# Optimization experiments

Hardware: AMD Instinct MI355X
Metric: run time of the kernel (lower is better)

The kernel has to match this reference:

```python
import jax, jax.numpy as jnp
import numpy as np

H, W, C, HEADS = 28, 28, 512, 16
N = H * W
FF = 4 * C
DH = C // HEADS
NUM_REL = (2 * H - 1) * W + (2 * W - 1) + 1  # max relative index + 1 (source table is under-sized; see notes)


def _relative_indices():
    ys, xs = np.meshgrid(np.arange(H), np.arange(W), indexing='ij')
    py, px = ys.reshape(-1), xs.reshape(-1)
    # rel[q, k] = (y_k - y_q + H) * W + (x_k - x_q + W), matching the source loop
    rel = (py[None, :] - py[:, None] + H) * W + (px[None, :] - px[:, None] + W)
    return jnp.asarray(rel, dtype=jnp.int32)  # (N, N)


def setup_inputs() -> dict:
    key = jax.random.key(0)
    ks = jax.random.split(key, 9)
    g = lambda k, shape, s: (jax.random.normal(k, shape, jnp.float32) * s)
    return {
        'x': g(ks[0], (16, C, H, W), 1.0),
        'ln_w': jnp.ones((C,), jnp.float32),
        'ln_b': jnp.zeros((C,), jnp.float32),
        'Wq': g(ks[1], (C, C), 0.02), 'bq': jnp.zeros((C,), jnp.float32),
        'Wk': g(ks[2], (C, C), 0.02), 'bk': jnp.zeros((C,), jnp.float32),
        'Wv': g(ks[3], (C, C), 0.02), 'bv': jnp.zeros((C,), jnp.float32),
        'Wo': g(ks[4], (C, C), 0.02), 'bo': jnp.zeros((C,), jnp.float32),
        'rel_bias': g(ks[5], (HEADS, NUM_REL), 0.02),
        'W1': g(ks[6], (C, FF), 0.02), 'b1': jnp.zeros((FF,), jnp.float32),
        'W2': g(ks[7], (FF, C), 0.02), 'b2': jnp.zeros((C,), jnp.float32),
        'rel_idx': _relative_indices(),
    }


def reference(x, ln_w, ln_b, Wq, bq, Wk, bk, Wv, bv, Wo, bo, rel_bias, W1, b1, W2, b2, rel_idx):
    b = x.shape[0]
    xc = jnp.transpose(x, (0, 2, 3, 1)).reshape(b, N, C)  # b n c
    # LayerNorm over channels (per spatial position)
    mu = xc.mean(-1, keepdims=True)
    var = jnp.mean(jnp.square(xc - mu), -1, keepdims=True)
    xn = (xc - mu) * jax.lax.rsqrt(var + 1e-5) * ln_w + ln_b

    split = lambda t: t.reshape(b, N, HEADS, DH).transpose(0, 2, 1, 3)  # b h n d
    q = split(xn @ Wq + bq)
    k = split(xn @ Wk + bk)
    v = split(xn @ Wv + bv)

    bias = rel_bias[:, rel_idx]  # gather -> (heads, n, n)
    scores = jnp.einsum('bhnd,bhmd->bhnm', q, k) + bias[None]  # no 1/sqrt(d), faithful to source
    attn = jax.nn.softmax(scores, axis=-1)
    out = jnp.einsum('bhnm,bhmd->bhnd', attn, v)
    out = out.transpose(0, 2, 1, 3).reshape(b, N, C) @ Wo + bo

    x1 = xc + out  # skip (Identity) + attention branch
    ff = jax.nn.gelu(x1 @ W1 + b1, approximate=False) @ W2 + b2
    x2 = x1 + ff
    return x2.reshape(b, H, W, C).transpose(0, 3, 1, 2)  # back to b c h w
```

## Files before the change

kernel.cpp:

```cpp
#include <hip/hip_runtime.h>
#include <hip/hip_bf16.h>
#include <math.h>
#include <stdint.h>


typedef __bf16 bf16;
typedef __attribute__((ext_vector_type(8))) __bf16 bf16x8;
typedef __attribute__((ext_vector_type(4))) __bf16 bf16x4;
typedef __attribute__((ext_vector_type(4))) float f32x4;

#define NN 784
#define CC 512
#define NHEADS 16
#define DHEAD 32
#define FFD 2048
#define NBATCH 16
#define NREL 1596
#define MFULL (NBATCH * NN)
#define PACKSZ ((size_t)6422528)

__global__ __launch_bounds__(256) void detect_dtype(const unsigned int* xw, int* flag)
{
  __shared__ int cnt[256];
  int plausible = 0;
  for (int i = threadIdx.x; i < 1024; i += 256) {
    unsigned w = xw[i];
    unsigned lo = w & 0xFFFFu;
    unsigned e = (lo >> 7) & 0xFFu;
    if (lo == 0u || (e >= 90u && e <= 140u)) plausible++;
  }
  cnt[threadIdx.x] = plausible;
  __syncthreads();
  if (threadIdx.x == 0) {
    int tot = 0;
    for (int i = 0; i < 256; i++) tot += cnt[i];
    flag[0] = (tot >= 768) ? 1 : 0;
  }
}


__global__ __launch_bounds__(256) void transpose_split(
    const float* __restrict__ W, bf16* __restrict__ th, bf16* __restrict__ tl,
    int K, int Nout, int roff, const int* __restrict__ flag)
{
  if (flag[0] != 0) return;
  __shared__ float tile[32][33];
  int n0 = blockIdx.x * 32, k0 = blockIdx.y * 32;
  int tx = threadIdx.x & 31, ty = threadIdx.x >> 5;
  #pragma unroll
  for (int r = 0; r < 32; r += 8)
    tile[ty + r][tx] = W[(size_t)(k0 + ty + r) * Nout + n0 + tx];
  __syncthreads();
  #pragma unroll
  for (int r = 0; r < 32; r += 8) {
    float v = tile[tx][ty + r];
    bf16 h = (bf16)v;
    float lo = v - (float)h;
    size_t idx = (size_t)(roff + n0 + ty + r) * K + k0 + tx;
    th[idx] = h;
    tl[idx] = (bf16)lo;
  }
}

__global__ __launch_bounds__(256) void ln_single(
    const float* __restrict__ x, const float* __restrict__ lnw,
    const float* __restrict__ lnb, bf16* __restrict__ xh,
    const int* __restrict__ flag)
{
  if (flag[0] != 0) return;
  int bn = blockIdx.x;
  int b = bn / NN, n = bn - b * NN;
  const float* xb = x + (size_t)b * CC * NN + n;
  int t = threadIdx.x;
  float v0 = xb[(size_t)t * NN];
  float v1 = xb[(size_t)(t + 256) * NN];
  float s = v0 + v1, ss = v0 * v0 + v1 * v1;
  #pragma unroll
  for (int m = 32; m >= 1; m >>= 1) {
    s  += __shfl_xor(s,  m);
    ss += __shfl_xor(ss, m);
  }
  __shared__ float red[2][4];
  int w = t >> 6, l = t & 63;
  if (l == 0) { red[0][w] = s; red[1][w] = ss; }
  __syncthreads();
  float S  = red[0][0] + red[0][1] + red[0][2] + red[0][3];
  float SS = red[1][0] + red[1][1] + red[1][2] + red[1][3];
  float mu  = S * (1.f / 512.f);
  float var = SS * (1.f / 512.f) - mu * mu;
  float rstd = rsqrtf(var + 1e-5f);
  size_t o = (size_t)bn * CC;
  xh[o + t]       = (bf16)(((v0 - mu) * rstd) * lnw[t]       + lnb[t]);
  xh[o + t + 256] = (bf16)(((v1 - mu) * rstd) * lnw[t + 256] + lnb[t + 256]);
}

template <int NOUT, int KD, int ACT, int RESM, int OUTM>
__global__ __launch_bounds__(256) void gemm2(
    const bf16* __restrict__ A,
    const bf16* __restrict__ Bh, const bf16* __restrict__ Bl,
    const float* __restrict__ bias_q, const float* __restrict__ bias_k,
    const float* __restrict__ bias_v,
    float* __restrict__ outf, bf16* __restrict__ out_hi, bf16* __restrict__ out_lo,
    const float* __restrict__ extra_f, const bf16* __restrict__ ex_hi,
    const bf16* __restrict__ ex_lo,
    int M, const int* __restrict__ flag)
{
  if (flag[0] != 0) return;
  __shared__ bf16 sA [128 * 32];
  __shared__ bf16 sBh[128 * 32];
  __shared__ bf16 sBl[128 * 32];
  const int t = threadIdx.x;
  const int lane = t & 63;
  const int w = t >> 6;
  const int wr = w >> 1, wc = w & 1;
  const int lr = lane & 15, kg = lane >> 4;

  int wg = blockIdx.y * gridDim.x + blockIdx.x;
  const int nwg = gridDim.x * gridDim.y;
  if ((nwg & 7) == 0) {
    const int cpx = nwg >> 3;
    wg = (wg & 7) * cpx + (wg >> 3);
  }
  const int tile_n = (wg % gridDim.x) * 128;
  const int tile_m = (wg / gridDim.x) * 128;

  f32x4 acc[4][4];
  #pragma unroll
  for (int m = 0; m < 4; m++)
    #pragma unroll
    for (int n = 0; n < 4; n++) acc[m][n] = (f32x4)0.f;

  const int s0 = t, s1 = t + 256;
  int ar0 = tile_m + (s0 >> 2); if (ar0 >= M) ar0 = M - 1;
  int ar1 = tile_m + (s1 >> 2); if (ar1 >= M) ar1 = M - 1;
  const int br0 = tile_n + (s0 >> 2);
  const int br1 = tile_n + (s1 >> 2);
  const int ac0 = (s0 & 3) * 8, ac1 = (s1 & 3) * 8;

  for (int k0 = 0; k0 < KD; k0 += 32) {
    const size_t a0 = (size_t)ar0 * KD + k0 + ac0;
    const size_t a1 = (size_t)ar1 * KD + k0 + ac1;
    const size_t b0 = (size_t)br0 * KD + k0 + ac0;
    const size_t b1 = (size_t)br1 * KD + k0 + ac1;
    __builtin_amdgcn_global_load_lds(
        (const __attribute__((address_space(1))) void*)(A + a0),
        (__attribute__((address_space(3))) void*)(sA + s0 * 8), 16, 0, 0);
    __builtin_amdgcn_global_load_lds(
        (const __attribute__((address_space(1))) void*)(A + a1),
        (__attribute__((address_space(3))) void*)(sA + s1 * 8), 16, 0, 0);
    __builtin_amdgcn_global_load_lds(
        (const __attribute__((address_space(1))) void*)(Bh + b0),
        (__attribute__((address_space(3))) void*)(sBh + s0 * 8), 16, 0, 0);
    __builtin_amdgcn_global_load_lds(
        (const __attribute__((address_space(1))) void*)(Bh + b1),
        (__attribute__((address_space(3))) void*)(sBh + s1 * 8), 16, 0, 0);
    __builtin_amdgcn_global_load_lds(
        (const __attribute__((address_space(1))) void*)(Bl + b0),
        (__attribute__((address_space(3))) void*)(sBl + s0 * 8), 16, 0, 0);
    __builtin_amdgcn_global_load_lds(
        (const __attribute__((address_space(1))) void*)(Bl + b1),
        (__attribute__((address_space(3))) void*)(sBl + s1 * 8), 16, 0, 0);
    __syncthreads();
    bf16x8 af[4], bh[4], bl[4];
    #pragma unroll
    for (int m = 0; m < 4; m++) {
      const int off = (wr * 64 + m * 16 + lr) * 32 + kg * 8;
      af[m] = *(const bf16x8*)(sA + off);
    }
    #pragma unroll
    for (int n = 0; n < 4; n++) {
      const int off = (wc * 64 + n * 16 + lr) * 32 + kg * 8;
      bh[n] = *(const bf16x8*)(sBh + off);
      bl[n] = *(const bf16x8*)(sBl + off);
    }
    #pragma unroll
    for (int m = 0; m < 4; m++)
      #pragma unroll
      for (int n = 0; n < 4; n++) {
        acc[m][n] = __builtin_amdgcn_mfma_f32_16x16x32_bf16(af[m], bh[n], acc[m][n], 0, 0, 0);
        acc[m][n] = __builtin_amdgcn_mfma_f32_16x16x32_bf16(af[m], bl[n], acc[m][n], 0, 0, 0);
      }
    __syncthreads();
  }

  #pragma unroll
  for (int m = 0; m < 4; m++) {
    const int r0 = tile_m + wr * 64 + m * 16 + kg * 4;
    #pragma unroll
    for (int n = 0; n < 4; n++) {
      const int cg = tile_n + wc * 64 + n * 16 + lr;
      float bv;
      if (OUTM == 5) {
        const int reg2 = cg >> 9;
        const float* bp = reg2 == 0 ? bias_q : (reg2 == 1 ? bias_k : bias_v);
        bv = bp[cg & 511];
      } else {
        bv = bias_q[cg];
      }
      #pragma unroll
      for (int j = 0; j < 4; j++) {
        const int rg = r0 + j;
        if (rg >= M) continue;
        float vacc = acc[m][n][j] + bv;
        if (ACT == 1) vacc = 0.5f * vacc * (1.f + erff(vacc * 0.70710678118654752f));
        if (RESM == 1) {
          int bl_ = rg / NN, nn = rg - bl_ * NN;
          vacc += extra_f[((size_t)bl_ * CC + cg) * NN + nn];
        }
        if (RESM == 2) {
          size_t ei = (size_t)rg * CC + cg;
          vacc += (float)ex_hi[ei] + (float)ex_lo[ei];
        }
        if (OUTM == 3) {
          size_t oi = (size_t)rg * NOUT + cg;
          bf16 h = (bf16)vacc;
          out_hi[oi] = h;
          out_lo[oi] = (bf16)(vacc - (float)h);
        } else if (OUTM == 4) {
          int bl_ = rg / NN, nn = rg - bl_ * NN;
          outf[((size_t)bl_ * CC + cg) * NN + nn] = vacc;
        } else if (OUTM == 6) {
          out_hi[(size_t)rg * NOUT + cg] = (bf16)vacc;
        } else if (OUTM == 5) {
          const int reg2 = cg >> 9;
          const int c = cg & 511;
          const int hh = c >> 5, dd = c & 31;
          const int bl_ = rg / NN, nn = rg - bl_ * NN;
          const int bh_ = bl_ * NHEADS + hh;
          bf16 h = (bf16)vacc;
          if (reg2 == 0) {
            out_hi[((size_t)bh_ * NN + nn) * 32 + dd] = h;
          } else if (reg2 == 1) {
            out_hi[PACKSZ + ((size_t)bh_ * NN + nn) * 32 + dd] = h;
          } else {
            out_hi[2 * PACKSZ + ((size_t)bh_ * 32 + dd) * NN + nn] = h;
          }
        }
      }
    }
  }
}

__global__ __launch_bounds__(256) void attn_mfma(
    const bf16* __restrict__ pack, const float* __restrict__ relb,
    bf16* __restrict__ o_out, const int* __restrict__ flag)
{
  if (flag[0] != 0) return;
  const int h = blockIdx.y, b = blockIdx.z;
  __shared__ float biasLds[NREL];
  for (int i = threadIdx.x; i < NREL; i += 256) biasLds[i] = relb[(size_t)h * NREL + i];
  __syncthreads();
  const int w = threadIdx.x >> 6, lane = threadIdx.x & 63;
  const int qtile = blockIdx.x * 4 + w;
  if (qtile >= 49) return;
  const int kg = lane >> 4, lq = lane & 15;
  const int qg = qtile * 16 + lq;
  const int bh = b * NHEADS + h;
  const bf16* Q  = pack;
  const bf16* K  = pack + PACKSZ;
  const bf16* Vt = pack + 2 * PACKSZ;
  __shared__ bf16 Plds[4][16][72];

  const bf16x8 qf = *(const bf16x8*)(Q + ((size_t)bh * NN + qg) * 32 + kg * 8);

  float m = -1e30f, l = 0.f;
  f32x4 o0 = (f32x4)0.f, o1 = (f32x4)0.f;
  const float* bb = biasLds + 812 - qg;
  const size_t vrow0 = ((size_t)bh * 32 + lq) * NN;
  const size_t vrow1 = ((size_t)bh * 32 + 16 + lq) * NN;

  for (int c = 0; c < 12; c++) {
    const int c0 = c * 64;
    f32x4 st[4];
    #pragma unroll
    for (int t = 0; t < 4; t++) {
      const int kvr = c0 + t * 16 + lq;
      const bf16x8 kf = *(const bf16x8*)(K + ((size_t)bh * NN + kvr) * 32 + kg * 8);
      st[t] = __builtin_amdgcn_mfma_f32_16x16x32_bf16(kf, qf, (f32x4)0.f, 0, 0, 0);
    }
    float cm = -1e30f;
    #pragma unroll
    for (int t = 0; t < 4; t++)
      #pragma unroll
      for (int r = 0; r < 4; r++) {
        st[t][r] += bb[c0 + t * 16 + 4 * kg + r];
        cm = fmaxf(cm, st[t][r]);
      }
    cm = fmaxf(cm, __shfl_xor(cm, 16));
    cm = fmaxf(cm, __shfl_xor(cm, 32));
    const float mn = fmaxf(m, cm);
    const float al = __expf(m - mn);
    m = mn;
    float cl = 0.f;
    #pragma unroll
    for (int t = 0; t < 4; t++) {
      bf16x4 pk;
      #pragma unroll
      for (int r = 0; r < 4; r++) {
        float p = __expf(st[t][r] - m);
        bf16 pb = (bf16)p;
        pk[r] = pb;
        cl += (float)pb;
      }
      *(bf16x4*)(&Plds[w][lq][t * 16 + 4 * kg]) = pk;
    }
    cl += __shfl_xor(cl, 16);
    cl += __shfl_xor(cl, 32);
    l = l * al + cl;
    #pragma unroll
    for (int r = 0; r < 4; r++) {
      const float ar = __shfl(al, (lane & 48) | (kg * 4 + r));
      o0[r] *= ar; o1[r] *= ar;
    }
    #pragma unroll
    for (int s2 = 0; s2 < 2; s2++) {
      const bf16x8 pa = *(const bf16x8*)(&Plds[w][lq][s2 * 32 + kg * 8]);
      const bf16x8 v0 = *(const bf16x8*)(Vt + vrow0 + c0 + s2 * 32 + kg * 8);
      const bf16x8 v1 = *(const bf16x8*)(Vt + vrow1 + c0 + s2 * 32 + kg * 8);
      o0 = __builtin_amdgcn_mfma_f32_16x16x32_bf16(pa, v0, o0, 0, 0, 0);
      o1 = __builtin_amdgcn_mfma_f32_16x16x32_bf16(pa, v1, o1, 0, 0, 0);
    }
  }

  {
    const int c0 = 768;
    const int kvr = c0 + lq;
    const bf16x8 kf = *(const bf16x8*)(K + ((size_t)bh * NN + kvr) * 32 + kg * 8);
    f32x4 a = __builtin_amdgcn_mfma_f32_16x16x32_bf16(kf, qf, (f32x4)0.f, 0, 0, 0);
    float cm = -1e30f;
    #pragma unroll
    for (int r = 0; r < 4; r++) {
      a[r] += bb[c0 + 4 * kg + r];
      cm = fmaxf(cm, a[r]);
    }
    cm = fmaxf(cm, __shfl_xor(cm, 16));
    cm = fmaxf(cm, __shfl_xor(cm, 32));
    const float mn = fmaxf(m, cm);
    const float al = __expf(m - mn);
    m = mn;
    float cl = 0.f;
    bf16x4 pk, zk;
    #pragma unroll
    for (int r = 0; r < 4; r++) {
      float p = __expf(a[r] - m);
      bf16 pb = (bf16)p;
      pk[r] = pb;
      zk[r] = (bf16)0.f;
      cl += (float)pb;
    }
    *(bf16x4*)(&Plds[w][lq][4 * kg]) = pk;
    *(bf16x4*)(&Plds[w][lq][16 + 4 * kg]) = zk;
    cl += __shfl_xor(cl, 16);
    cl += __shfl_xor(cl, 32);
    l = l * al + cl;
    #pragma unroll
    for (int r = 0; r < 4; r++) {
      const float ar = __shfl(al, (lane & 48) | (kg * 4 + r));
      o0[r] *= ar; o1[r] *= ar;
    }
    bf16x8 vz;
    #pragma unroll
    for (int e = 0; e < 8; e++) vz[e] = (bf16)0.f;
    const int voff = c0 + (kg < 2 ? kg * 8 : 0);
    bf16x8 v0 = *(const bf16x8*)(Vt + vrow0 + voff);
    bf16x8 v1 = *(const bf16x8*)(Vt + vrow1 + voff);
    if (kg >= 2) { v0 = vz; v1 = vz; }
    const bf16x8 pa = *(const bf16x8*)(&Plds[w][lq][kg * 8]);
    o0 = __builtin_amdgcn_mfma_f32_16x16x32_bf16(pa, v0, o0, 0, 0, 0);
    o1 = __builtin_amdgcn_mfma_f32_16x16x32_bf16(pa, v1, o1, 0, 0, 0);
  }

  const float inv = 1.f / l;
  #pragma unroll
  for (int r = 0; r < 4; r++) {
    const float ir = __shfl(inv, (lane & 48) | (kg * 4 + r));
    const int rq = qtile * 16 + kg * 4 + r;
    const size_t oi = ((size_t)b * NN + rq) * CC + h * DHEAD;
    o_out[oi + lq]      = (bf16)(o0[r] * ir);
    o_out[oi + 16 + lq] = (bf16)(o1[r] * ir);
  }
}

static void run_fast_fp32(void* const* d_in, void* d_out, char* base,
                          const int* flag, hipStream_t stream)
{
  const float* x    = (const float*)d_in[0];
  const float* lnw  = (const float*)d_in[1];
  const float* lnb  = (const float*)d_in[2];
  const float* Wq   = (const float*)d_in[3];
  const float* bq   = (const float*)d_in[4];
  const float* Wk   = (const float*)d_in[5];
  const float* bk   = (const float*)d_in[6];
  const float* Wv   = (const float*)d_in[7];
  const float* bv   = (const float*)d_in[8];
  const float* Wo   = (const float*)d_in[9];
  const float* bo   = (const float*)d_in[10];
  const float* relb = (const float*)d_in[11];
  const float* W1   = (const float*)d_in[12];
  const float* b1   = (const float*)d_in[13];
  const float* W2   = (const float*)d_in[14];
  const float* b2   = (const float*)d_in[15];
  float* outp = (float*)d_out;

  bf16* WqkvT_h = (bf16*)(base);
  bf16* WqkvT_l = WqkvT_h + (size_t)1536 * 512;
  bf16* WoT_h   = WqkvT_l + (size_t)1536 * 512;
  bf16* WoT_l   = WoT_h   + (size_t)512 * 512;
  bf16* W1T_h   = WoT_l   + (size_t)512 * 512;
  bf16* W1T_l   = W1T_h   + (size_t)2048 * 512;
  bf16* W2T_h   = W1T_l   + (size_t)2048 * 512;
  bf16* W2T_l   = W2T_h   + (size_t)512 * 2048;
  bf16* xn   = (bf16*)(base + 12582912);
  bf16* qkvp = (bf16*)(base + 25427968);
  bf16* x1_h = (bf16*)(base + 25427968);
  bf16* x1_l = (bf16*)(base + 38273024);
  bf16* ff   = (bf16*)(base + 51118080);
  bf16* at   = xn;

  transpose_split<<<dim3(16, 16), 256, 0, stream>>>(Wq, WqkvT_h, WqkvT_l, 512, 512, 0, flag);
  transpose_split<<<dim3(16, 16), 256, 0, stream>>>(Wk, WqkvT_h, WqkvT_l, 512, 512, 512, flag);
  transpose_split<<<dim3(16, 16), 256, 0, stream>>>(Wv, WqkvT_h, WqkvT_l, 512, 512, 1024, flag);
  transpose_split<<<dim3(16, 16), 256, 0, stream>>>(Wo, WoT_h, WoT_l, 512, 512, 0, flag);
  transpose_split<<<dim3(64, 16), 256, 0, stream>>>(W1, W1T_h, W1T_l, 512, 2048, 0, flag);
  transpose_split<<<dim3(16, 64), 256, 0, stream>>>(W2, W2T_h, W2T_l, 2048, 512, 0, flag);

  const int M = MFULL;
  const int gm = M / 128;

  ln_single<<<dim3(M), 256, 0, stream>>>(x, lnw, lnb, xn, flag);

  gemm2<1536, 512, 0, 0, 5><<<dim3(12, gm), 256, 0, stream>>>(
      xn, WqkvT_h, WqkvT_l, bq, bk, bv,
      (float*)nullptr, qkvp, (bf16*)nullptr,
      (const float*)nullptr, (const bf16*)nullptr, (const bf16*)nullptr,
      M, flag);

  attn_mfma<<<dim3(13, NHEADS, NBATCH), 256, 0, stream>>>(qkvp, relb, at, flag);

  gemm2<512, 512, 0, 1, 3><<<dim3(4, gm), 256, 0, stream>>>(
      at, WoT_h, WoT_l, bo, (const float*)nullptr, (const float*)nullptr,
      (float*)nullptr, x1_h, x1_l,
      x, (const bf16*)nullptr, (const bf16*)nullptr,
      M, flag);

  gemm2<2048, 512, 1, 0, 6><<<dim3(16, gm), 256, 0, stream>>>(
      x1_h, W1T_h, W1T_l, b1, (const float*)nullptr, (const float*)nullptr,
      (float*)nullptr, ff, (bf16*)nullptr,
      (const float*)nullptr, (const bf16*)nullptr, (const bf16*)nullptr,
      M, flag);

  gemm2<512, 2048, 0, 2, 4><<<dim3(4, gm), 256, 0, stream>>>(
      ff, W2T_h, W2T_l, b2, (const float*)nullptr, (const float*)nullptr,
      outp, (bf16*)nullptr, (bf16*)nullptr,
      (const float*)nullptr, x1_h, x1_l,
      M, flag);
}

template <typename T, int WANT>
__global__ __launch_bounds__(256) void ln_naive(
    const T* __restrict__ x, const T* __restrict__ lnw, const T* __restrict__ lnb,
    T* __restrict__ xn, const int* __restrict__ flag)
{
  if (flag[0] != WANT) return;
  int bn = blockIdx.x;
  int b = bn / NN, n = bn - b * NN;
  const T* xb = x + (size_t)b * CC * NN + n;
  int t = threadIdx.x;
  float v0 = (float)xb[(size_t)t * NN];
  float v1 = (float)xb[(size_t)(t + 256) * NN];
  float s = v0 + v1, ss = v0 * v0 + v1 * v1;
  #pragma unroll
  for (int m = 32; m >= 1; m >>= 1) {
    s  += __shfl_xor(s,  m);
    ss += __shfl_xor(ss, m);
  }
  __shared__ float red[2][4];
  int w = t >> 6, l = t & 63;
  if (l == 0) { red[0][w] = s; red[1][w] = ss; }
  __syncthreads();
  float S  = red[0][0] + red[0][1] + red[0][2] + red[0][3];
  float SS = red[1][0] + red[1][1] + red[1][2] + red[1][3];
  float mu  = S * (1.f / 512.f);
  float var = SS * (1.f / 512.f) - mu * mu;
  float rstd = rsqrtf(var + 1e-5f);
  T* o = xn + (size_t)bn * CC;
  o[t]       = (T)(((v0 - mu) * rstd) * (float)lnw[t]       + (float)lnb[t]);
  o[t + 256] = (T)(((v1 - mu) * rstd) * (float)lnw[t + 256] + (float)lnb[t + 256]);
}

template <typename T, int NOUT, int KD, int ACT, int RESM, int OUTM, int WANT>
__global__ __launch_bounds__(256) void gemm_naive(
    const T* __restrict__ A, const T* __restrict__ W, const T* __restrict__ bias,
    T* __restrict__ out, const T* __restrict__ extra, const int* __restrict__ flag)
{
  if (flag[0] != WANT) return;
  __shared__ float a_t[16][17];
  __shared__ float w_t[16][17];
  int tx = threadIdx.x & 15, ty = threadIdx.x >> 4;
  int m0 = blockIdx.y * 16, bz = blockIdx.z;
  int mg = m0 + ty;
  int jg = blockIdx.x * 16 + tx;
  int ar = mg < NN ? mg : NN - 1;
  const T* Ab = A + (size_t)bz * NN * KD;
  float acc = 0.f;
  for (int k0 = 0; k0 < KD; k0 += 16) {
    a_t[ty][tx] = (float)Ab[(size_t)ar * KD + k0 + tx];
    w_t[ty][tx] = (float)W[(size_t)(k0 + ty) * NOUT + jg];
    __syncthreads();
    #pragma unroll
    for (int kk = 0; kk < 16; kk++)
      acc += a_t[ty][kk] * w_t[kk][tx];
    __syncthreads();
  }
  if (mg >= NN) return;
  acc += (float)bias[jg];
  if (ACT == 1) acc = 0.5f * acc * (1.f + erff(acc * 0.70710678118654752f));
  if (RESM == 1) acc += (float)extra[((size_t)bz * CC + jg) * NN + mg];
  if (RESM == 2) acc += (float)extra[((size_t)bz * NN + mg) * CC + jg];
  if (OUTM == 0) out[((size_t)bz * NN + mg) * NOUT + jg] = (T)acc;
  else           out[((size_t)bz * NOUT + jg) * NN + mg] = (T)acc;
}

template <typename T, int WANT>
__global__ __launch_bounds__(256) void attn_naive(
    const T* __restrict__ q, const T* __restrict__ k, const T* __restrict__ v,
    const T* __restrict__ rel_bias, const int* __restrict__ rel_idx,
    T* __restrict__ attn_out, const int* __restrict__ flag)
{
  if (flag[0] != WANT) return;
  int i = blockIdx.x * 256 + threadIdx.x;
  int h = blockIdx.y, b = blockIdx.z;
  if (i >= NN) return;
  const T* qr = q + ((size_t)b * NN + i) * CC + h * DHEAD;
  float qv[DHEAD];
  #pragma unroll
  for (int d = 0; d < DHEAD; d++) qv[d] = (float)qr[d];
  const int* ridx = rel_idx + (size_t)i * NN;
  const T* rb = rel_bias + (size_t)h * NREL;
  const T* kb = k + (size_t)b * NN * CC + h * DHEAD;
  const T* vb = v + (size_t)b * NN * CC + h * DHEAD;

  float m = -1e30f;
  for (int j = 0; j < NN; j++) {
    const T* kr = kb + (size_t)j * CC;
    float s = 0.f;
    #pragma unroll
    for (int d = 0; d < DHEAD; d++) s += qv[d] * (float)kr[d];
    s += (float)rb[ridx[j]];
    m = fmaxf(m, s);
  }
  float l = 0.f;
  float o[DHEAD];
  #pragma unroll
  for (int d = 0; d < DHEAD; d++) o[d] = 0.f;
  for (int j = 0; j < NN; j++) {
    const T* kr = kb + (size_t)j * CC;
    float s = 0.f;
    #pragma unroll
    for (int d = 0; d < DHEAD; d++) s += qv[d] * (float)kr[d];
    s += (float)rb[ridx[j]];
    float p = __expf(s - m);
    l += p;
    const T* vr = vb + (size_t)j * CC;
    #pragma unroll
    for (int d = 0; d < DHEAD; d++) o[d] += p * (float)vr[d];
  }
  float inv = 1.f / l;
  T* op = attn_out + ((size_t)b * NN + i) * CC + h * DHEAD;
  #pragma unroll
  for (int d = 0; d < DHEAD; d++) op[d] = (T)(o[d] * inv);
}

template <typename T, int WANT>
static void run_pipeline(void* const* d_in, void* d_out, char* buf, int Bc,
                         const int* flag, hipStream_t stream)
{
  const T* x    = (const T*)d_in[0];
  const T* lnw  = (const T*)d_in[1];
  const T* lnb  = (const T*)d_in[2];
  const T* Wq   = (const T*)d_in[3];
  const T* bq   = (const T*)d_in[4];
  const T* Wk   = (const T*)d_in[5];
  const T* bk   = (const T*)d_in[6];
  const T* Wv   = (const T*)d_in[7];
  const T* bv   = (const T*)d_in[8];
  const T* Wo   = (const T*)d_in[9];
  const T* bo   = (const T*)d_in[10];
  const T* relb = (const T*)d_in[11];
  const T* W1   = (const T*)d_in[12];
  const T* b1   = (const T*)d_in[13];
  const T* W2   = (const T*)d_in[14];
  const T* b2   = (const T*)d_in[15];
  const int* reli = (const int*)d_in[16];
  T* outp = (T*)d_out;

  const size_t TOK = (size_t)NN * CC;
  T* xn  = (T*)(buf);
  T* qb  = (T*)(buf + (size_t)Bc * TOK * 4);
  T* kb  = (T*)(buf + 2 * (size_t)Bc * TOK * 4);
  T* vb  = (T*)(buf + 3 * (size_t)Bc * TOK * 4);
  T* ff1 = (T*)(buf + 4 * (size_t)Bc * TOK * 4);
  T* attn_out = xn;
  T* x1 = qb;

  for (int c0 = 0; c0 < NBATCH; c0 += Bc) {
    const T* xc   = x    + (size_t)c0 * CC * NN;
    T*       outc = outp + (size_t)c0 * CC * NN;
    ln_naive<T, WANT><<<dim3(Bc * NN), 256, 0, stream>>>(xc, lnw, lnb, xn, flag);
    gemm_naive<T, CC, CC, 0, 0, 0, WANT><<<dim3(32, 49, Bc), 256, 0, stream>>>(xn, Wq, bq, qb, (const T*)nullptr, flag);
    gemm_naive<T, CC, CC, 0, 0, 0, WANT><<<dim3(32, 49, Bc), 256, 0, stream>>>(xn, Wk, bk, kb, (const T*)nullptr, flag);
    gemm_naive<T, CC, CC, 0, 0, 0, WANT><<<dim3(32, 49, Bc), 256, 0, stream>>>(xn, Wv, bv, vb, (const T*)nullptr, flag);
    attn_naive<T, WANT><<<dim3(4, NHEADS, Bc), 256, 0, stream>>>(qb, kb, vb, relb, reli, attn_out, flag);
    gemm_naive<T, CC, CC, 0, 1, 0, WANT><<<dim3(32, 49, Bc), 256, 0, stream>>>(attn_out, Wo, bo, x1, xc, flag);
    gemm_naive<T, FFD, CC, 1, 0, 0, WANT><<<dim3(128, 49, Bc), 256, 0, stream>>>(x1, W1, b1, ff1, (const T*)nullptr, flag);
    gemm_naive<T, CC, FFD, 0, 2, 1, WANT><<<dim3(32, 49, Bc), 256, 0, stream>>>(ff1, W2, b2, outc, x1, flag);
  }
}

extern "C" void kernel_launch(void* const* d_in, const int* in_sizes, int n_in,
                              void* d_out, int out_size, void* d_ws, size_t ws_size,
                              hipStream_t stream)
{
  int* flag = (int*)d_ws;
  char* base = (char*)d_ws + 256;
  size_t avail = ws_size > 256 ? ws_size - 256 : 0;

  const size_t REQ_FAST = 102498304;
  const size_t PB16 = (size_t)(4 * NN * CC + NN * FFD) * 2;
  const size_t PB32 = (size_t)(4 * NN * CC + NN * FFD) * 4;

  detect_dtype<<<dim3(1), 256, 0, stream>>>((const unsigned int*)d_in[0], flag);

  if (avail >= REQ_FAST) {
    run_fast_fp32(d_in, d_out, base, flag, stream);
  } else {
    int Bc32 = 1;
    for (int c : {16, 8, 4, 2}) {
      if ((size_t)c * PB32 <= avail) { Bc32 = c; break; }
    }
    run_pipeline<float, 0>(d_in, d_out, base, Bc32, flag, stream);
  }

  int Bc16 = 1;
  for (int c : {16, 8, 4, 2}) {
    if ((size_t)c * PB16 <= avail) { Bc16 = c; break; }
  }
  run_pipeline<bf16, 1>(d_in, d_out, base, Bc16, flag, stream);
}
```

Before: 615.2 us.

## Double-buffer GEMM LDS tiles and merge weight transposes into one launch

The GEMM main loop now keeps two LDS buffers and issues the global-to-LDS loads for the next K slice before computing on the current one, with one barrier per iteration instead of two. The six weight transpose/split launches are merged into a single launch that picks its matrix from the block index. The aim is to hide global load latency behind the MFMA work and to cut per-launch overhead. LDS use per block doubles to about 48KB, which may lower occupancy.

```diff
diff --git a/kernel.cpp b/kernel.cpp
--- a/kernel.cpp
+++ b/kernel.cpp
@@ -39,13 +39,28 @@
 }
 
 
-__global__ __launch_bounds__(256) void transpose_split(
-    const float* __restrict__ W, bf16* __restrict__ th, bf16* __restrict__ tl,
-    int K, int Nout, int roff, const int* __restrict__ flag)
+__global__ __launch_bounds__(256) void transpose_split_all(
+    const float* __restrict__ Wq, const float* __restrict__ Wk,
+    const float* __restrict__ Wv, const float* __restrict__ Wo,
+    const float* __restrict__ W1, const float* __restrict__ W2,
+    bf16* __restrict__ WqkvT_h, bf16* __restrict__ WqkvT_l,
+    bf16* __restrict__ WoT_h,   bf16* __restrict__ WoT_l,
+    bf16* __restrict__ W1T_h,   bf16* __restrict__ W1T_l,
+    bf16* __restrict__ W2T_h,   bf16* __restrict__ W2T_l,
+    const int* __restrict__ flag)
 {
   if (flag[0] != 0) return;
+  int id = blockIdx.x;
+  const float* W; bf16 *th, *tl; int K, Nout, roff, nx;
+  if (id < 256)       { W = Wq; th = WqkvT_h; tl = WqkvT_l; K = 512;  Nout = 512;  roff = 0;    nx = 16; }
+  else if (id < 512)  { W = Wk; th = WqkvT_h; tl = WqkvT_l; K = 512;  Nout = 512;  roff = 512;  nx = 16; id -= 256; }
+  else if (id < 768)  { W = Wv; th = WqkvT_h; tl = WqkvT_l; K = 512;  Nout = 512;  roff = 1024; nx = 16; id -= 512; }
+  else if (id < 1024) { W = Wo; th = WoT_h;   tl = WoT_l;   K = 512;  Nout = 512;  roff = 0;    nx = 16; id -= 768; }
+  else if (id < 2048) { W = W1; th = W1T_h;   tl = W1T_l;   K = 512;  Nout = 2048; roff = 0;    nx = 64; id -= 1024; }
+  else                { W = W2; th = W2T_h;   tl = W2T_l;   K = 2048; Nout = 512;  roff = 0;    nx = 16; id -= 2048; }
+  const int n0 = (id % nx) * 32, k0 = (id / nx) * 32;
+
   __shared__ float tile[32][33];
-  int n0 = blockIdx.x * 32, k0 = blockIdx.y * 32;
   int tx = threadIdx.x & 31, ty = threadIdx.x >> 5;
   #pragma unroll
   for (int r = 0; r < 32; r += 8)
@@ -106,9 +121,9 @@
     int M, const int* __restrict__ flag)
 {
   if (flag[0] != 0) return;
-  __shared__ bf16 sA [128 * 32];
-  __shared__ bf16 sBh[128 * 32];
-  __shared__ bf16 sBl[128 * 32];
+  __shared__ bf16 sA [2][128 * 32];
+  __shared__ bf16 sBh[2][128 * 32];
+  __shared__ bf16 sBl[2][128 * 32];
   const int t = threadIdx.x;
   const int lane = t & 63;
   const int w = t >> 6;
@@ -136,42 +151,58 @@
   const int br0 = tile_n + (s0 >> 2);
   const int br1 = tile_n + (s1 >> 2);
   const int ac0 = (s0 & 3) * 8, ac1 = (s1 & 3) * 8;
-
+  const size_t a0 = (size_t)ar0 * KD + ac0;
+  const size_t a1 = (size_t)ar1 * KD + ac1;
+  const size_t b0 = (size_t)br0 * KD + ac0;
+  const size_t b1 = (size_t)br1 * KD + ac1;
+
+  #define STAGE(BUF, KO)                                                      \
+    do {                                                                      \
+      __builtin_amdgcn_global_load_lds(                                       \
+          (const __attribute__((address_space(1))) void*)(A + a0 + (KO)),     \
+          (__attribute__((address_space(3))) void*)(sA[BUF] + s0 * 8), 16, 0, 0); \
+      __builtin_amdgcn_global_load_lds(                                       \
+          (const __attribute__((address_space(1))) void*)(A + a1 + (KO)),     \
+          (__attribute__((address_space(3))) void*)(sA[BUF] + s1 * 8), 16, 0, 0); \
+      __builtin_amdgcn_global_load_lds(                                       \
+          (const __attribute__((address_space(1))) void*)(Bh + b0 + (KO)),    \
+          (__attribute__((address_space(3))) void*)(sBh[BUF] + s0 * 8), 16, 0, 0); \
+      __builtin_amdgcn_global_load_lds(                                       \
+          (const __attribute__((address_space(1))) void*)(Bh + b1 + (KO)),    \
+          (__attribute__((address_space(3))) void*)(sBh[BUF] + s1 * 8), 16, 0, 0); \
+      __builtin_amdgcn_global_load_lds(                                       \
+          (const __attribute__((address_space(1))) void*)(Bl + b0 + (KO)),    \
+          (__attribute__((address_space(3))) void*)(sBl[BUF] + s0 * 8), 16, 0, 0); \
+      __builtin_amdgcn_global_load_lds(                                       \
+          (const __attribute__((address_space(1))) void*)(Bl + b1 + (KO)),    \
+          (__attribute__((address_space(3))) void*)(sBl[BUF] + s1 * 8), 16, 0, 0); \
+    } while (0)
+
+  STAGE(0, 0);
+  asm volatile("s_waitcnt vmcnt(0)" ::: "memory");
+  __builtin_amdgcn_sched_barrier(0);
+  __builtin_amdgcn_s_barrier();
+  __builtin_amdgcn_sched_barrier(0);
+
+  int cur = 0;
   for (int k0 = 0; k0 < KD; k0 += 32) {
-    const size_t a0 = (size_t)ar0 * KD + k0 + ac0;
-    const size_t a1 = (size_t)ar1 * KD + k0 + ac1;
-    const size_t b0 = (size_t)br0 * KD + k0 + ac0;
-    const size_t b1 = (size_t)br1 * KD + k0 + ac1;
-    __builtin_amdgcn_global_load_lds(
-        (const __attribute__((address_space(1))) void*)(A + a0),
-        (__attribute__((address_space(3))) void*)(sA + s0 * 8), 16, 0, 0);
-    __builtin_amdgcn_global_load_lds(
-        (const __attribute__((address_space(1))) void*)(A + a1),
-        (__attribute__((address_space(3))) void*)(sA + s1 * 8), 16, 0, 0);
-    __builtin_amdgcn_global_load_lds(
-        (const __attribute__((address_space(1))) void*)(Bh + b0),
-        (__attribute__((address_space(3))) void*)(sBh + s0 * 8), 16, 0, 0);
-    __builtin_amdgcn_global_load_lds(
-        (const __attribute__((address_space(1))) void*)(Bh + b1),
-        (__attribute__((address_space(3))) void*)(sBh + s1 * 8), 16, 0, 0);
-    __builtin_amdgcn_global_load_lds(
-        (const __attribute__((address_space(1))) void*)(Bl + b0),
-        (__attribute__((address_space(3))) void*)(sBl + s0 * 8), 16, 0, 0);
-    __builtin_amdgcn_global_load_lds(
-        (const __attribute__((address_space(1))) void*)(Bl + b1),
-        (__attribute__((address_space(3))) void*)(sBl + s1 * 8), 16, 0, 0);
-    __syncthreads();
+    if (k0 + 32 < KD) {
+      if (cur) STAGE(0, k0 + 32); else STAGE(1, k0 + 32);
+    }
+    const bf16* pA  = sA [cur];
+    const bf16* pBh = sBh[cur];
+    const bf16* pBl = sBl[cur];
     bf16x8 af[4], bh[4], bl[4];
     #pragma unroll
     for (int m = 0; m < 4; m++) {
       const int off = (wr * 64 + m * 16 + lr) * 32 + kg * 8;
-      af[m] = *(const bf16x8*)(sA + off);
+      af[m] = *(const bf16x8*)(pA + off);
     }
     #pragma unroll
     for (int n = 0; n < 4; n++) {
       const int off = (wc * 64 + n * 16 + lr) * 32 + kg * 8;
-      bh[n] = *(const bf16x8*)(sBh + off);
-      bl[n] = *(const bf16x8*)(sBl + off);
+      bh[n] = *(const bf16x8*)(pBh + off);
+      bl[n] = *(const bf16x8*)(pBl + off);
     }
     #pragma unroll
     for (int m = 0; m < 4; m++)
@@ -180,8 +211,13 @@
         acc[m][n] = __builtin_amdgcn_mfma_f32_16x16x32_bf16(af[m], bh[n], acc[m][n], 0, 0, 0);
         acc[m][n] = __builtin_amdgcn_mfma_f32_16x16x32_bf16(af[m], bl[n], acc[m][n], 0, 0, 0);
       }
-    __syncthreads();
-  }
+    asm volatile("s_waitcnt vmcnt(0)" ::: "memory");
+    __builtin_amdgcn_sched_barrier(0);
+    __builtin_amdgcn_s_barrier();
+    __builtin_amdgcn_sched_barrier(0);
+    cur ^= 1;
+  }
+  #undef STAGE
 
   #pragma unroll
   for (int m = 0; m < 4; m++) {
@@ -417,12 +453,9 @@
   bf16* ff   = (bf16*)(base + 51118080);
   bf16* at   = xn;
 
-  transpose_split<<<dim3(16, 16), 256, 0, stream>>>(Wq, WqkvT_h, WqkvT_l, 512, 512, 0, flag);
-  transpose_split<<<dim3(16, 16), 256, 0, stream>>>(Wk, WqkvT_h, WqkvT_l, 512, 512, 512, flag);
-  transpose_split<<<dim3(16, 16), 256, 0, stream>>>(Wv, WqkvT_h, WqkvT_l, 512, 512, 1024, flag);
-  transpose_split<<<dim3(16, 16), 256, 0, stream>>>(Wo, WoT_h, WoT_l, 512, 512, 0, flag);
-  transpose_split<<<dim3(64, 16), 256, 0, stream>>>(W1, W1T_h, W1T_l, 512, 2048, 0, flag);
-  transpose_split<<<dim3(16, 64), 256, 0, stream>>>(W2, W2T_h, W2T_l, 2048, 512, 0, flag);
+  transpose_split_all<<<dim3(3072), 256, 0, stream>>>(
+      Wq, Wk, Wv, Wo, W1, W2,
+      WqkvT_h, WqkvT_l, WoT_h, WoT_l, W1T_h, W1T_l, W2T_h, W2T_l, flag);
 
   const int M = MFULL;
   const int gm = M / 128;
```

After: 578.8 us. 5.9% less time.
